# Optimization experiments

Hardware: AMD Instinct MI355X
Metric: run time of the kernel (lower is better)

Reference implementation:

```python
import jax, jax.numpy as jnp
import numpy as np

N_NODES = 50000
N_EDGES = 800000
IN_CH, HID, OUT_CH = 128, 256, 40


def setup_inputs() -> dict:
    key = jax.random.key(0)
    ks = jax.random.split(key, 10)
    x = jax.random.normal(ks[0], (N_NODES, IN_CH), dtype=jnp.float32)
    edge_index = jax.random.randint(ks[1], (2, N_EDGES), 0, N_NODES, dtype=jnp.int64)
    s = 0.05  # weight init scale
    return {
        "x": x,
        "edge_index": edge_index,
        "W1a": jax.random.normal(ks[2], (IN_CH, HID), dtype=jnp.float32) * s,
        "b1a": jnp.zeros((HID,), jnp.float32),
        "W2a": jax.random.normal(ks[3], (HID, HID), dtype=jnp.float32) * s,
        "b2a": jnp.zeros((HID,), jnp.float32),
        "W1b": jax.random.normal(ks[4], (HID, HID), dtype=jnp.float32) * s,
        "b1b": jnp.zeros((HID,), jnp.float32),
        "W2b": jax.random.normal(ks[5], (HID, HID), dtype=jnp.float32) * s,
        "b2b": jnp.zeros((HID,), jnp.float32),
        "Wlin": jax.random.normal(ks[6], (HID * 2, OUT_CH), dtype=jnp.float32) * s,
        "blin": jnp.zeros((OUT_CH,), jnp.float32),
    }


def _gin_conv(h, src, dst, W1, b1, W2, b2):
    # sum-aggregate messages h[src] into destination nodes, eps = 0
    agg = jax.ops.segment_sum(h[src], dst, num_segments=N_NODES)
    z = h + agg
    z = jnp.maximum(z @ W1 + b1, 0.0) @ W2 + b2  # 2-layer MLP
    return z


def reference(x, edge_index, W1a, b1a, W2a, b2a, W1b, b1b, W2b, b2b, Wlin, blin):
    src, dst = edge_index[0], edge_index[1]
    h1 = jnp.maximum(_gin_conv(x, src, dst, W1a, b1a, W2a, b2a), 0.0)
    h2 = jnp.maximum(_gin_conv(h1, src, dst, W1b, b1b, W2b, b2b), 0.0)
    h_cat = jnp.concatenate([h1, h2], axis=1)  # [N, 2*HID]
    logits = h_cat @ Wlin + blin
    return jax.nn.log_softmax(logits, axis=1)
```

## Files before the change

### kernel.cpp

```cpp
#include <hip/hip_runtime.h>
#include <math.h>

#define N_NODES 50000
#define N_EDGES 800000
#define IN_CH 128
#define HID 256
#define OUT_CH 40
#define GRP 6250
#define NCHUNK 64
#define TS 264

typedef unsigned short u16;
typedef unsigned char u8;
typedef __attribute__((ext_vector_type(8))) short bf16x8;
typedef __attribute__((ext_vector_type(8))) unsigned short u16x8;
typedef __attribute__((ext_vector_type(4))) float f32x4;
typedef __attribute__((ext_vector_type(2))) float f32x2;

__device__ __forceinline__ float bf2f(u16 u) {
    union { unsigned int i; float f; } v; v.i = ((unsigned int)u) << 16; return v.f;
}
__device__ __forceinline__ u16 f2bf(float f) {
    union { float f; unsigned int i; } v; v.f = f;
    unsigned int x = v.i;
    x += 0x7fffu + ((x >> 16) & 1u);
    return (u16)(x >> 16);
}

#define GLOBAL_AS __attribute__((address_space(1)))
#define LDS_AS __attribute__((address_space(3)))
__device__ __forceinline__ void async_cp16(const void* g, void* l) {
    __builtin_amdgcn_global_load_lds((const GLOBAL_AS unsigned int*)g,
                                     (LDS_AS unsigned int*)l, 16, 0, 0);
}

__device__ __forceinline__ void pack_w(
    const float* __restrict__ in, u16* __restrict__ out, int K, int N, int c)
{
    for (int k = threadIdx.x; k < K; k += 256) {
        int kk32 = k >> 5, quad = (k >> 3) & 3, e = k & 7;
        size_t base = (((size_t)c * (K >> 5) + kk32) * 64 + quad * 16) * 8 + e;
#pragma unroll
        for (int li = 0; li < 16; li++) {
            int n = c * 16 + li;
            float v = (n < N) ? in[(size_t)k * N + n] : 0.f;
            out[base + (size_t)li * 8] = f2bf(v);
        }
    }
}

__global__ __launch_bounds__(256) void prep_fused(
    const float* __restrict__ x, u16* __restrict__ xb, u8* __restrict__ xf8,
    const int* __restrict__ ei, u16* __restrict__ e16,
    const float* __restrict__ W1a, const float* __restrict__ W2a,
    const float* __restrict__ W1b, const float* __restrict__ W2b,
    const float* __restrict__ Wlin,
    u16* __restrict__ W1aPk, u16* __restrict__ W2aPk,
    u16* __restrict__ W1bPk, u16* __restrict__ W2bPk, u16* __restrict__ WlinPk)
{
    int b = blockIdx.x;
    if (b < 6250) {
        int i = b * 256 + threadIdx.x;
        float4 v = ((const float4*)x)[i];
        ushort4 o;
        o.x = f2bf(v.x); o.y = f2bf(v.y); o.z = f2bf(v.z); o.w = f2bf(v.w);
        ((ushort4*)xb)[i] = o;
        int p = __builtin_amdgcn_cvt_pk_fp8_f32(v.x, v.y, 0, false);
        p = __builtin_amdgcn_cvt_pk_fp8_f32(v.z, v.w, p, true);
        ((unsigned int*)xf8)[i] = (unsigned int)p;
    } else if (b < 7813) {
        int i = (b - 6250) * 256 + threadIdx.x;
        if (i < (2 * N_EDGES) / 4) {
            int4 v = ((const int4*)ei)[i];
            ushort4 o;
            o.x = (u16)v.x; o.y = (u16)v.y; o.z = (u16)v.z; o.w = (u16)v.w;
            ((ushort4*)e16)[i] = o;
        }
    } else {
        int t = b - 7813;
        if (t < 16)       pack_w(W1a, W1aPk, IN_CH, HID, t);
        else if (t < 32)  pack_w(W2a, W2aPk, HID, HID, t - 16);
        else if (t < 48)  pack_w(W1b, W1bPk, HID, HID, t - 32);
        else if (t < 64)  pack_w(W2b, W2bPk, HID, HID, t - 48);
        else              pack_w(Wlin, WlinPk, 2 * HID, OUT_CH, t - 64);
    }
}

__global__ __launch_bounds__(256) void hist_priv(
    const u16* __restrict__ dst16, u16* __restrict__ partial)
{
    __shared__ int hist[GRP];
    const int b = blockIdx.x;
    const int g = b & 7;
    const int sub = b >> 3;
    const int lo = g * GRP;
    const int CH = N_EDGES / NCHUNK;
    for (int i = threadIdx.x; i < GRP; i += 256) hist[i] = 0;
    __syncthreads();
    const ushort4* dsts = (const ushort4*)(dst16 + sub * CH);
    for (int k = threadIdx.x; k < CH / 4; k += 256) {
        ushort4 d = dsts[k];
        int r0 = (int)d.x - lo, r1 = (int)d.y - lo;
        int r2 = (int)d.z - lo, r3 = (int)d.w - lo;
        if ((unsigned)r0 < (unsigned)GRP) atomicAdd(&hist[r0], 1);
        if ((unsigned)r1 < (unsigned)GRP) atomicAdd(&hist[r1], 1);
        if ((unsigned)r2 < (unsigned)GRP) atomicAdd(&hist[r2], 1);
        if ((unsigned)r3 < (unsigned)GRP) atomicAdd(&hist[r3], 1);
    }
    __syncthreads();
    u16* po = partial + (size_t)b * GRP;
    for (int i = threadIdx.x; i < GRP; i += 256) po[i] = (u16)hist[i];
}

__global__ __launch_bounds__(256) void scan1(
    const u16* __restrict__ partial, int* __restrict__ excl,
    int* __restrict__ partials_out)
{
    __shared__ int lds[256];
    const int tid = threadIdx.x;
    const int base = blockIdx.x * 1024 + tid * 4;
    int v[4]; int s = 0;
#pragma unroll
    for (int i = 0; i < 4; i++) {
        int idx = base + i;
        int d = 0;
        if (idx < N_NODES) {
            int g = idx / GRP;
            int off = idx - g * GRP;
#pragma unroll
            for (int sub = 0; sub < NCHUNK; sub++)
                d += partial[(size_t)(sub * 8 + g) * GRP + off];
        }
        v[i] = d;
        s += d;
    }
    lds[tid] = s;
    __syncthreads();
    for (int off = 1; off < 256; off <<= 1) {
        int t = (tid >= off) ? lds[tid - off] : 0;
        __syncthreads();
        lds[tid] += t;
        __syncthreads();
    }
    int run = lds[tid] - s;
#pragma unroll
    for (int i = 0; i < 4; i++) {
        int idx = base + i;
        if (idx < N_NODES) excl[idx] = run;
        run += v[i];
    }
    if (tid == 255) partials_out[blockIdx.x] = lds[255];
}

__global__ __launch_bounds__(256) void scan3(
    int* __restrict__ excl, const int* __restrict__ partials,
    int* __restrict__ cursor, int nPart)
{
    __shared__ int bp[64];
    const int tid = threadIdx.x;
    if (tid < 64) {
        int orig = (tid < nPart) ? partials[tid] : 0;
        int v = orig;
#pragma unroll
        for (int off = 1; off < 64; off <<= 1) {
            int t = __shfl_up(v, off, 64);
            if (tid >= off) v += t;
        }
        bp[tid] = v - orig;
    }
    __syncthreads();
    int idx = blockIdx.x * 256 + tid;
    if (idx < N_NODES) {
        int r = excl[idx] + bp[idx >> 10];
        excl[idx] = r;
        cursor[idx] = r;
    }
}

__global__ __launch_bounds__(256) void csr_fill(
    const u16* __restrict__ src16, const u16* __restrict__ dst16,
    int* __restrict__ cursor, u16* __restrict__ csr_src)
{
    const int g = blockIdx.x & 7;
    const int c = blockIdx.x >> 3;
    const int lo = g * GRP, hi = lo + GRP;
    const int base = c * 2048;
#pragma unroll
    for (int i = 0; i < 8; i++) {
        int e = base + i * 256 + threadIdx.x;
        if (e < N_EDGES) {
            int d = dst16[e];
            if (d >= lo && d < hi) {
                int pos = atomicAdd(&cursor[d], 1);
                csr_src[pos] = src16[e];
            }
        }
    }
}


__global__ __launch_bounds__(256) void gather_agg_f8_128(
    const u16* __restrict__ feat_bf, const u8* __restrict__ feat_f8,
    const int* __restrict__ row_ptr, const int* __restrict__ row_end,
    const u16* __restrict__ csr_src, u16* __restrict__ out)
{
    const int tid = threadIdx.x;
    const int lane = tid & 63;
    const int wv = tid >> 6;
    const int li = lane & 7;
    int node = blockIdx.x * 32 + wv * 8 + (lane >> 3);
    const bool valid = node < N_NODES;
    if (!valid) node = N_NODES - 1;

    int j = row_ptr[node];
    int deg = valid ? (row_end[node] - j) : 0;

    float acc[16];
    {
        u16x8 s0 = *(const u16x8*)(feat_bf + (size_t)node * IN_CH + li * 16);
        u16x8 s1 = *(const u16x8*)(feat_bf + (size_t)node * IN_CH + li * 16 + 8);
#pragma unroll
        for (int q = 0; q < 8; q++) { acc[q] = bf2f(s0[q]); acc[8 + q] = bf2f(s1[q]); }
    }

    int maxdeg = deg;
#pragma unroll
    for (int off = 8; off < 64; off <<= 1)
        maxdeg = max(maxdeg, __shfl_xor(maxdeg, off, 64));

    for (int it = 0; it < maxdeg; it += 2) {
        int4 g0 = {0, 0, 0, 0}, g1 = {0, 0, 0, 0};
        if (it < deg)
            g0 = *(const int4*)(feat_f8 + (size_t)csr_src[j + it] * IN_CH + li * 16);
        if (it + 1 < deg)
            g1 = *(const int4*)(feat_f8 + (size_t)csr_src[j + it + 1] * IN_CH + li * 16);
#pragma unroll
        for (int q = 0; q < 4; q++) {
            int w0 = (&g0.x)[q], w1 = (&g1.x)[q];
            f32x2 l0 = __builtin_amdgcn_cvt_pk_f32_fp8(w0, false);
            f32x2 h0 = __builtin_amdgcn_cvt_pk_f32_fp8(w0, true);
            f32x2 l1 = __builtin_amdgcn_cvt_pk_f32_fp8(w1, false);
            f32x2 h1 = __builtin_amdgcn_cvt_pk_f32_fp8(w1, true);
            acc[q * 4 + 0] += l0.x + l1.x;
            acc[q * 4 + 1] += l0.y + l1.y;
            acc[q * 4 + 2] += h0.x + h1.x;
            acc[q * 4 + 3] += h0.y + h1.y;
        }
    }

    if (valid) {
        u16x8 o0, o1;
#pragma unroll
        for (int q = 0; q < 8; q++) { o0[q] = f2bf(acc[q]); o1[q] = f2bf(acc[8 + q]); }
        *(u16x8*)(out + (size_t)node * IN_CH + li * 16) = o0;
        *(u16x8*)(out + (size_t)node * IN_CH + li * 16 + 8) = o1;
    }
}

__global__ __launch_bounds__(256) void gather_agg_f8_256(
    const u16* __restrict__ feat_bf, const u8* __restrict__ feat_f8,
    const int* __restrict__ row_ptr, const int* __restrict__ row_end,
    const u16* __restrict__ csr_src, u16* __restrict__ out)
{
    const int tid = threadIdx.x;
    const int lane = tid & 63;
    const int wv = tid >> 6;
    const int li = lane & 15;
    const int node = blockIdx.x * 16 + wv * 4 + (lane >> 4);

    int j = row_ptr[node];
    int deg = row_end[node] - j;

    float acc[16];
    {
        u16x8 s0 = *(const u16x8*)(feat_bf + (size_t)node * HID + li * 16);
        u16x8 s1 = *(const u16x8*)(feat_bf + (size_t)node * HID + li * 16 + 8);
#pragma unroll
        for (int q = 0; q < 8; q++) { acc[q] = bf2f(s0[q]); acc[8 + q] = bf2f(s1[q]); }
    }

    int maxdeg = deg;
#pragma unroll
    for (int off = 16; off < 64; off <<= 1)
        maxdeg = max(maxdeg, __shfl_xor(maxdeg, off, 64));

    for (int it = 0; it < maxdeg; it += 2) {
        int4 g0 = {0, 0, 0, 0}, g1 = {0, 0, 0, 0};
        if (it < deg)
            g0 = *(const int4*)(feat_f8 + (size_t)csr_src[j + it] * HID + li * 16);
        if (it + 1 < deg)
            g1 = *(const int4*)(feat_f8 + (size_t)csr_src[j + it + 1] * HID + li * 16);
#pragma unroll
        for (int q = 0; q < 4; q++) {
            int w0 = (&g0.x)[q], w1 = (&g1.x)[q];
            f32x2 l0 = __builtin_amdgcn_cvt_pk_f32_fp8(w0, false);
            f32x2 h0 = __builtin_amdgcn_cvt_pk_f32_fp8(w0, true);
            f32x2 l1 = __builtin_amdgcn_cvt_pk_f32_fp8(w1, false);
            f32x2 h1 = __builtin_amdgcn_cvt_pk_f32_fp8(w1, true);
            acc[q * 4 + 0] += l0.x + l1.x;
            acc[q * 4 + 1] += l0.y + l1.y;
            acc[q * 4 + 2] += h0.x + h1.x;
            acc[q * 4 + 3] += h0.y + h1.y;
        }
    }

    u16x8 o0, o1;
#pragma unroll
    for (int q = 0; q < 8; q++) { o0[q] = f2bf(acc[q]); o1[q] = f2bf(acc[8 + q]); }
    *(u16x8*)(out + (size_t)node * HID + li * 16) = o0;
    *(u16x8*)(out + (size_t)node * HID + li * 16 + 8) = o1;
}

__global__ __launch_bounds__(256, 4) void mlp_fused(
    const u16* __restrict__ A, int K1,
    const u16* __restrict__ W1pk, const float* __restrict__ b1,
    const u16* __restrict__ W2pk, const float* __restrict__ b2,
    u16* __restrict__ out, u8* __restrict__ outF8, int M)
{
    __shared__ u16 SB[64 * TS];

    const int tid = threadIdx.x;
    const int lane = tid & 63;
    const int wid = tid >> 6;
    const int li = lane & 15;
    const int quad = lane >> 4;
    const int koff = quad * 8;
    const int row0 = blockIdx.x * 64;
    const int KB1 = K1 >> 5;
    const int rsh = (K1 == 256) ? 9 : 8;

    {
        const u8* Ag = (const u8*)(A + (size_t)row0 * K1);
        const int rounds = K1 >> 5;
        for (int j = 0; j < rounds; j++) {
            int L = (j * 256 + tid) * 16;
            int G = L ^ (((L >> rsh) & 7) << 4);
            async_cp16(Ag + G, (u8*)SB + L);
        }
    }

    f32x4 acc[4][4];
#pragma unroll
    for (int i = 0; i < 4; i++)
#pragma unroll
        for (int j = 0; j < 4; j++) acc[i][j] = (f32x4){0.f, 0.f, 0.f, 0.f};

    __syncthreads();

    for (int kk = 0; kk < K1; kk += 32) {
        const int kk32 = kk >> 5;
        bf16x8 af[4], wf[4];
#pragma unroll
        for (int t = 0; t < 4; t++) {
            int row = t * 16 + li;
            int bo = row * (K1 * 2) + (kk + koff) * 2;
            bo ^= (row & 7) << 4;
            af[t] = *(const bf16x8*)((const u8*)SB + bo);
        }
#pragma unroll
        for (int t = 0; t < 4; t++)
            wf[t] = *(const bf16x8*)(W1pk +
                (((size_t)(wid * 4 + t) * KB1 + kk32) * 64 + lane) * 8);
#pragma unroll
        for (int mt = 0; mt < 4; mt++)
#pragma unroll
            for (int nt = 0; nt < 4; nt++)
                acc[mt][nt] = __builtin_amdgcn_mfma_f32_16x16x32_bf16(
                    af[mt], wf[nt], acc[mt][nt], 0, 0, 0);
    }
    __syncthreads();

#pragma unroll
    for (int nt = 0; nt < 4; nt++) {
        int col = wid * 64 + nt * 16 + li;
        float bv = b1[col];
#pragma unroll
        for (int mt = 0; mt < 4; mt++) {
#pragma unroll
            for (int reg = 0; reg < 4; reg++) {
                int row = mt * 16 + quad * 4 + reg;
                float v = fmaxf(acc[mt][nt][reg] + bv, 0.f);
                SB[row * TS + col] = f2bf(v);
                acc[mt][nt][reg] = 0.f;
            }
        }
    }
    __syncthreads();

    for (int kk = 0; kk < HID; kk += 32) {
        const int kk32 = kk >> 5;
        bf16x8 af[4], wf[4];
#pragma unroll
        for (int t = 0; t < 4; t++)
            af[t] = *(const bf16x8*)(SB + (t * 16 + li) * TS + kk + koff);
#pragma unroll
        for (int t = 0; t < 4; t++)
            wf[t] = *(const bf16x8*)(W2pk +
                (((size_t)(wid * 4 + t) * 8 + kk32) * 64 + lane) * 8);
#pragma unroll
        for (int mt = 0; mt < 4; mt++)
#pragma unroll
            for (int nt = 0; nt < 4; nt++)
                acc[mt][nt] = __builtin_amdgcn_mfma_f32_16x16x32_bf16(
                    af[mt], wf[nt], acc[mt][nt], 0, 0, 0);
    }

    __syncthreads();
#pragma unroll
    for (int nt = 0; nt < 4; nt++) {
        int col = wid * 64 + nt * 16 + li;
        float bv = b2[col];
#pragma unroll
        for (int mt = 0; mt < 4; mt++) {
#pragma unroll
            for (int reg = 0; reg < 4; reg++) {
                int row = mt * 16 + quad * 4 + reg;
                float v = fmaxf(acc[mt][nt][reg] + bv, 0.f);
                SB[row * TS + col] = f2bf(v);
            }
        }
    }
    __syncthreads();
#pragma unroll
    for (int it = 0; it < 8; it++) {
        int flat = it * 4096 + tid * 16;
        int r = flat >> 9;
        int cu = (flat & 511) >> 1;
        int row = row0 + r;
        if (row < M) {
            u16x8 v = *(const u16x8*)(SB + r * TS + cu);
            *(u16x8*)(out + (size_t)row * HID + cu) = v;
            if (outF8 != nullptr) {
                int p0 = __builtin_amdgcn_cvt_pk_fp8_f32(bf2f(v[0]), bf2f(v[1]), 0, false);
                p0 = __builtin_amdgcn_cvt_pk_fp8_f32(bf2f(v[2]), bf2f(v[3]), p0, true);
                int p1 = __builtin_amdgcn_cvt_pk_fp8_f32(bf2f(v[4]), bf2f(v[5]), 0, false);
                p1 = __builtin_amdgcn_cvt_pk_fp8_f32(bf2f(v[6]), bf2f(v[7]), p1, true);
                int2 pv; pv.x = p0; pv.y = p1;
                *(int2*)(outF8 + (size_t)row * HID + cu) = pv;
            }
        }
    }
}

__global__ __launch_bounds__(256, 6) void gemm_mfma(
    const u16* __restrict__ A, const u16* __restrict__ Acat, int Ksplit, int ldA,
    const u16* __restrict__ Bpk, const float* __restrict__ bias,
    float* __restrict__ out, int M, int K)
{
    const int tid = threadIdx.x;
    const int lane = tid & 63;
    const int wid = tid >> 6;
    const int li = lane & 15;
    const int quad = lane >> 4;
    const int koff = quad * 8;
    const int row0 = blockIdx.x * 64 + wid * 16;

    f32x4 acc[3];
#pragma unroll
    for (int i = 0; i < 3; i++) acc[i] = (f32x4){0.f, 0.f, 0.f, 0.f};

    int r = row0 + li;
    const int arow = (r < M) ? r : (M - 1);
    const int KB = K >> 5;

#define LD_G(AF, BF, KK)                                                      \
    {   const u16* Ab = ((KK) >= Ksplit) ? Acat : A;                          \
        const int kb = ((KK) >= Ksplit) ? ((KK) - Ksplit) : (KK);             \
        AF = *(const bf16x8*)(Ab + (size_t)arow * ldA + kb + koff);           \
        _Pragma("unroll")                                                     \
        for (int t = 0; t < 3; t++)                                           \
            BF[t] = *(const bf16x8*)(Bpk +                                    \
                (((size_t)t * KB + ((KK) >> 5)) * 64 + lane) * 8); }
#define MFMA3(AF, BF)                                                         \
    {   _Pragma("unroll")                                                     \
        for (int nt = 0; nt < 3; nt++)                                        \
            acc[nt] = __builtin_amdgcn_mfma_f32_16x16x32_bf16(                \
                AF, BF[nt], acc[nt], 0, 0, 0); }

    {
        bf16x8 a0, b0[3], a1, b1v[3];
        LD_G(a0, b0, 0);
        for (int kk = 0; kk < K; kk += 64) {
            LD_G(a1, b1v, kk + 32);
            MFMA3(a0, b0);
            if (kk + 64 < K) LD_G(a0, b0, kk + 64);
            MFMA3(a1, b1v);
        }
    }
#undef LD_G
#undef MFMA3

    float b0v = bias[li];
    float b1s = bias[16 + li];
    float b2s = (li < 8) ? bias[32 + li] : 0.f;
#pragma unroll
    for (int reg = 0; reg < 4; reg++) {
        int row = row0 + quad * 4 + reg;
        float v0 = acc[0][reg] + b0v;
        float v1 = acc[1][reg] + b1s;
        float v2 = (li < 8) ? (acc[2][reg] + b2s) : -INFINITY;
        float m = fmaxf(fmaxf(v0, v1), v2);
#pragma unroll
        for (int off = 1; off < 16; off <<= 1)
            m = fmaxf(m, __shfl_xor(m, off, 64));
        float s = expf(v0 - m) + expf(v1 - m)
                + ((li < 8) ? expf(v2 - m) : 0.f);
#pragma unroll
        for (int off = 1; off < 16; off <<= 1)
            s += __shfl_xor(s, off, 64);
        float lg = m + logf(s);
        if (row < M) {
            out[(size_t)row * OUT_CH + li] = v0 - lg;
            out[(size_t)row * OUT_CH + 16 + li] = v1 - lg;
            if (li < 8) out[(size_t)row * OUT_CH + 32 + li] = v2 - lg;
        }
    }
}

extern "C" void kernel_launch(void* const* d_in, const int* in_sizes, int n_in,
                              void* d_out, int out_size, void* d_ws, size_t ws_size,
                              hipStream_t stream)
{
    const float* x    = (const float*)d_in[0];
    const int*   ei   = (const int*)d_in[1];
    const float* W1a  = (const float*)d_in[2];
    const float* b1a  = (const float*)d_in[3];
    const float* W2a  = (const float*)d_in[4];
    const float* b2a  = (const float*)d_in[5];
    const float* W1b  = (const float*)d_in[6];
    const float* b1b  = (const float*)d_in[7];
    const float* W2b  = (const float*)d_in[8];
    const float* b2b  = (const float*)d_in[9];
    const float* Wlin = (const float*)d_in[10];
    const float* blin = (const float*)d_in[11];
    float* out = (float*)d_out;

    const size_t R = (size_t)N_NODES * HID;
    u16* R0 = (u16*)d_ws;
    u16* R1 = R0 + R;
    u16* R2 = R1 + R;
    u16* R3 = R2 + R;
    u16* R4 = R3 + R;
    u16* xbf = R0;
    u16* zA  = R1;
    u16* partial = (u16*)R1;
    u8*  xf8 = (u8*)(R1 + (size_t)N_NODES * IN_CH);
    u8*  h1f8 = (u8*)R1;
    u16* h1  = R3;
    u16* zB  = R4;
    u16* h2  = R2;

    u16* wts = R4 + R;
    u16* W1aPk = wts;
    u16* W2aPk = W1aPk + 256 * 128;
    u16* W1bPk = W2aPk + 256 * 256;
    u16* W2bPk = W1bPk + 256 * 256;
    u16* WlinPk = W2bPk + 256 * 256;
    int* rowp   = (int*)(WlinPk + 128 * 512);
    int* cursor = rowp + N_NODES;
    int* part   = cursor + N_NODES;
    u16* csr    = (u16*)(part + 64);
    u16* e16    = csr + N_EDGES;
    u16* src16  = e16;
    u16* dst16  = e16 + N_EDGES;

    dim3 blk(256);
    const int scanBlocks = (N_NODES + 1023) / 1024;
    const int fillBlocks = 8 * ((N_EDGES + 2047) / 2048);
    const int agg128Blocks = (N_NODES + 31) / 32;
    const int agg256Blocks = N_NODES / 16;
    const int mlpBlocks  = (N_NODES + 63) / 64;
    const int gemmBlocks = (N_NODES + 63) / 64;

    prep_fused<<<7880, blk, 0, stream>>>(x, xbf, xf8, ei, e16,
                                         W1a, W2a, W1b, W2b, Wlin,
                                         W1aPk, W2aPk, W1bPk, W2bPk, WlinPk);
    hist_priv<<<8 * NCHUNK, blk, 0, stream>>>(dst16, partial);
    scan1<<<scanBlocks, blk, 0, stream>>>(partial, rowp, part);
    scan3<<<(N_NODES + 255) / 256, blk, 0, stream>>>(rowp, part, cursor, scanBlocks);
    csr_fill<<<fillBlocks, blk, 0, stream>>>(src16, dst16, cursor, csr);

    gather_agg_f8_128<<<agg128Blocks, blk, 0, stream>>>(xbf, xf8, rowp, cursor, csr, zA);
    mlp_fused<<<mlpBlocks, blk, 0, stream>>>(zA, IN_CH, W1aPk, b1a, W2aPk, b2a,
                                             h1, h1f8, N_NODES);

    gather_agg_f8_256<<<agg256Blocks, blk, 0, stream>>>(h1, h1f8, rowp, cursor, csr, zB);
    mlp_fused<<<mlpBlocks, blk, 0, stream>>>(zB, HID, W1bPk, b1b, W2bPk, b2b,
                                             h2, nullptr, N_NODES);

    gemm_mfma<<<gemmBlocks, blk, 0, stream>>>(h1, h2, HID, HID, WlinPk, blin,
                                              out, N_NODES, 2 * HID);
}
```

Before: 289.5 us.

## Unroll edge gather by four and double-buffer weight loads in fused MLP

The two gather-aggregate kernels now fetch four neighbor fp8 rows per iteration instead of two, which puts more independent global loads in flight per wave. The fused MLP kernel now software-pipelines its weight fragments through two register buffers, issuing the next k-step's global weight load before the MFMAs of the current step so load latency overlaps compute. The cost is higher register pressure, which under launch_bounds(256,4) could cause spills, plus a small change in the floating-point summation order.

```diff
diff --git a/kernel.cpp b/kernel.cpp
--- a/kernel.cpp
+++ b/kernel.cpp
@@ -228,23 +228,31 @@
     for (int off = 8; off < 64; off <<= 1)
         maxdeg = max(maxdeg, __shfl_xor(maxdeg, off, 64));
 
-    for (int it = 0; it < maxdeg; it += 2) {
-        int4 g0 = {0, 0, 0, 0}, g1 = {0, 0, 0, 0};
+    for (int it = 0; it < maxdeg; it += 4) {
+        int4 g0 = {0,0,0,0}, g1 = {0,0,0,0}, g2 = {0,0,0,0}, g3 = {0,0,0,0};
         if (it < deg)
             g0 = *(const int4*)(feat_f8 + (size_t)csr_src[j + it] * IN_CH + li * 16);
         if (it + 1 < deg)
             g1 = *(const int4*)(feat_f8 + (size_t)csr_src[j + it + 1] * IN_CH + li * 16);
+        if (it + 2 < deg)
+            g2 = *(const int4*)(feat_f8 + (size_t)csr_src[j + it + 2] * IN_CH + li * 16);
+        if (it + 3 < deg)
+            g3 = *(const int4*)(feat_f8 + (size_t)csr_src[j + it + 3] * IN_CH + li * 16);
 #pragma unroll
         for (int q = 0; q < 4; q++) {
-            int w0 = (&g0.x)[q], w1 = (&g1.x)[q];
+            int w0 = (&g0.x)[q], w1 = (&g1.x)[q], w2 = (&g2.x)[q], w3 = (&g3.x)[q];
             f32x2 l0 = __builtin_amdgcn_cvt_pk_f32_fp8(w0, false);
             f32x2 h0 = __builtin_amdgcn_cvt_pk_f32_fp8(w0, true);
             f32x2 l1 = __builtin_amdgcn_cvt_pk_f32_fp8(w1, false);
             f32x2 h1 = __builtin_amdgcn_cvt_pk_f32_fp8(w1, true);
-            acc[q * 4 + 0] += l0.x + l1.x;
-            acc[q * 4 + 1] += l0.y + l1.y;
-            acc[q * 4 + 2] += h0.x + h1.x;
-            acc[q * 4 + 3] += h0.y + h1.y;
+            f32x2 l2 = __builtin_amdgcn_cvt_pk_f32_fp8(w2, false);
+            f32x2 h2 = __builtin_amdgcn_cvt_pk_f32_fp8(w2, true);
+            f32x2 l3 = __builtin_amdgcn_cvt_pk_f32_fp8(w3, false);
+            f32x2 h3 = __builtin_amdgcn_cvt_pk_f32_fp8(w3, true);
+            acc[q * 4 + 0] += (l0.x + l1.x) + (l2.x + l3.x);
+            acc[q * 4 + 1] += (l0.y + l1.y) + (l2.y + l3.y);
+            acc[q * 4 + 2] += (h0.x + h1.x) + (h2.x + h3.x);
+            acc[q * 4 + 3] += (h0.y + h1.y) + (h2.y + h3.y);
         }
     }
 
@@ -284,23 +292,31 @@
     for (int off = 16; off < 64; off <<= 1)
         maxdeg = max(maxdeg, __shfl_xor(maxdeg, off, 64));
 
-    for (int it = 0; it < maxdeg; it += 2) {
-        int4 g0 = {0, 0, 0, 0}, g1 = {0, 0, 0, 0};
+    for (int it = 0; it < maxdeg; it += 4) {
+        int4 g0 = {0,0,0,0}, g1 = {0,0,0,0}, g2 = {0,0,0,0}, g3 = {0,0,0,0};
         if (it < deg)
             g0 = *(const int4*)(feat_f8 + (size_t)csr_src[j + it] * HID + li * 16);
         if (it + 1 < deg)
             g1 = *(const int4*)(feat_f8 + (size_t)csr_src[j + it + 1] * HID + li * 16);
+        if (it + 2 < deg)
+            g2 = *(const int4*)(feat_f8 + (size_t)csr_src[j + it + 2] * HID + li * 16);
+        if (it + 3 < deg)
+            g3 = *(const int4*)(feat_f8 + (size_t)csr_src[j + it + 3] * HID + li * 16);
 #pragma unroll
         for (int q = 0; q < 4; q++) {
-            int w0 = (&g0.x)[q], w1 = (&g1.x)[q];
+            int w0 = (&g0.x)[q], w1 = (&g1.x)[q], w2 = (&g2.x)[q], w3 = (&g3.x)[q];
             f32x2 l0 = __builtin_amdgcn_cvt_pk_f32_fp8(w0, false);
             f32x2 h0 = __builtin_amdgcn_cvt_pk_f32_fp8(w0, true);
             f32x2 l1 = __builtin_amdgcn_cvt_pk_f32_fp8(w1, false);
             f32x2 h1 = __builtin_amdgcn_cvt_pk_f32_fp8(w1, true);
-            acc[q * 4 + 0] += l0.x + l1.x;
-            acc[q * 4 + 1] += l0.y + l1.y;
-            acc[q * 4 + 2] += h0.x + h1.x;
-            acc[q * 4 + 3] += h0.y + h1.y;
+            f32x2 l2 = __builtin_amdgcn_cvt_pk_f32_fp8(w2, false);
+            f32x2 h2 = __builtin_amdgcn_cvt_pk_f32_fp8(w2, true);
+            f32x2 l3 = __builtin_amdgcn_cvt_pk_f32_fp8(w3, false);
+            f32x2 h3 = __builtin_amdgcn_cvt_pk_f32_fp8(w3, true);
+            acc[q * 4 + 0] += (l0.x + l1.x) + (l2.x + l3.x);
+            acc[q * 4 + 1] += (l0.y + l1.y) + (l2.y + l3.y);
+            acc[q * 4 + 2] += (h0.x + h1.x) + (h2.x + h3.x);
+            acc[q * 4 + 3] += (h0.y + h1.y) + (h2.y + h3.y);
         }
     }
 
@@ -345,28 +361,42 @@
 #pragma unroll
         for (int j = 0; j < 4; j++) acc[i][j] = (f32x4){0.f, 0.f, 0.f, 0.f};
 
-    __syncthreads();
-
-    for (int kk = 0; kk < K1; kk += 32) {
-        const int kk32 = kk >> 5;
-        bf16x8 af[4], wf[4];
-#pragma unroll
-        for (int t = 0; t < 4; t++) {
-            int row = t * 16 + li;
-            int bo = row * (K1 * 2) + (kk + koff) * 2;
-            bo ^= (row & 7) << 4;
-            af[t] = *(const bf16x8*)((const u8*)SB + bo);
-        }
-#pragma unroll
-        for (int t = 0; t < 4; t++)
-            wf[t] = *(const bf16x8*)(W1pk +
-                (((size_t)(wid * 4 + t) * KB1 + kk32) * 64 + lane) * 8);
-#pragma unroll
-        for (int mt = 0; mt < 4; mt++)
-#pragma unroll
-            for (int nt = 0; nt < 4; nt++)
-                acc[mt][nt] = __builtin_amdgcn_mfma_f32_16x16x32_bf16(
-                    af[mt], wf[nt], acc[mt][nt], 0, 0, 0);
+#define LDW(WF, WPK, KB, KK32)                                                \
+    {   _Pragma("unroll")                                                     \
+        for (int t = 0; t < 4; t++)                                           \
+            WF[t] = *(const bf16x8*)((WPK) +                                  \
+                (((size_t)(wid * 4 + t) * (KB) + (KK32)) * 64 + lane) * 8); }
+#define LDA1(AF, KK)                                                          \
+    {   _Pragma("unroll")                                                     \
+        for (int t = 0; t < 4; t++) {                                         \
+            int row = t * 16 + li;                                            \
+            int bo = row * (K1 * 2) + ((KK) + koff) * 2;                      \
+            bo ^= (row & 7) << 4;                                             \
+            AF[t] = *(const bf16x8*)((const u8*)SB + bo); } }
+#define LDA2(AF, KK)                                                          \
+    {   _Pragma("unroll")                                                     \
+        for (int t = 0; t < 4; t++)                                           \
+            AF[t] = *(const bf16x8*)(SB + (t * 16 + li) * TS + (KK) + koff); }
+#define MFMA16(AF, WF)                                                        \
+    {   _Pragma("unroll")                                                     \
+        for (int mt = 0; mt < 4; mt++)                                        \
+            _Pragma("unroll")                                                 \
+            for (int nt = 0; nt < 4; nt++)                                    \
+                acc[mt][nt] = __builtin_amdgcn_mfma_f32_16x16x32_bf16(        \
+                    AF[mt], WF[nt], acc[mt][nt], 0, 0, 0); }
+
+    bf16x8 wfA[4], wfB[4], af[4];
+
+    LDW(wfA, W1pk, KB1, 0);
+    __syncthreads();
+
+    for (int kk32 = 0; kk32 < KB1; kk32 += 2) {
+        LDW(wfB, W1pk, KB1, kk32 + 1);
+        LDA1(af, kk32 * 32);
+        MFMA16(af, wfA);
+        if (kk32 + 2 < KB1) LDW(wfA, W1pk, KB1, kk32 + 2);
+        LDA1(af, kk32 * 32 + 32);
+        MFMA16(af, wfB);
     }
     __syncthreads();
 
@@ -385,25 +415,21 @@
             }
         }
     }
-    __syncthreads();
-
-    for (int kk = 0; kk < HID; kk += 32) {
-        const int kk32 = kk >> 5;
-        bf16x8 af[4], wf[4];
-#pragma unroll
-        for (int t = 0; t < 4; t++)
-            af[t] = *(const bf16x8*)(SB + (t * 16 + li) * TS + kk + koff);
-#pragma unroll
-        for (int t = 0; t < 4; t++)
-            wf[t] = *(const bf16x8*)(W2pk +
-                (((size_t)(wid * 4 + t) * 8 + kk32) * 64 + lane) * 8);
-#pragma unroll
-        for (int mt = 0; mt < 4; mt++)
-#pragma unroll
-            for (int nt = 0; nt < 4; nt++)
-                acc[mt][nt] = __builtin_amdgcn_mfma_f32_16x16x32_bf16(
-                    af[mt], wf[nt], acc[mt][nt], 0, 0, 0);
-    }
+    LDW(wfA, W2pk, 8, 0);
+    __syncthreads();
+
+    for (int kk32 = 0; kk32 < 8; kk32 += 2) {
+        LDW(wfB, W2pk, 8, kk32 + 1);
+        LDA2(af, kk32 * 32);
+        MFMA16(af, wfA);
+        if (kk32 + 2 < 8) LDW(wfA, W2pk, 8, kk32 + 2);
+        LDA2(af, kk32 * 32 + 32);
+        MFMA16(af, wfB);
+    }
+#undef LDW
+#undef LDA1
+#undef LDA2
+#undef MFMA16
 
     __syncthreads();
 #pragma unroll
```

Result: no change. 286.5 us (-1.0%).
